# Kernel tuning notes

Hardware: AMD Instinct MI355X
Metric: run time of the kernel (lower is better)

Reference implementation:

```python
import jax, jax.numpy as jnp
import numpy as np

N_NODES = 50000
N_EDGES = 800000
IN_C = 128
OUT_C = 128
EDGE_F = 16
NEG_SLOPE = 0.2
BN_EPS = 1e-5


def setup_inputs() -> dict:
    key = jax.random.key(0)
    ks = jax.random.split(key, 8)
    x = jax.random.normal(ks[0], (N_NODES, IN_C), dtype=jnp.float32)
    edge_index = jax.random.randint(ks[1], (2, N_EDGES), 0, N_NODES, dtype=jnp.int64)
    edge_attr = jax.random.normal(ks[2], (N_EDGES, EDGE_F), dtype=jnp.float32)
    W = jax.random.normal(ks[3], (IN_C, OUT_C), dtype=jnp.float32) / np.sqrt(IN_C)
    att_src = jax.random.normal(ks[4], (OUT_C,), dtype=jnp.float32) / np.sqrt(OUT_C)
    att_dst = jax.random.normal(ks[5], (OUT_C,), dtype=jnp.float32) / np.sqrt(OUT_C)
    bias = jnp.zeros((OUT_C,), dtype=jnp.float32)
    gamma = jnp.ones((OUT_C,), dtype=jnp.float32)
    beta = jnp.zeros((OUT_C,), dtype=jnp.float32)
    return {"x": x, "edge_index": edge_index, "edge_attr": edge_attr, "W": W,
            "att_src": att_src, "att_dst": att_dst, "bias": bias,
            "gamma": gamma, "beta": beta}


def reference(x, edge_index, edge_attr, W, att_src, att_dst, bias, gamma, beta):
    # GATConv, heads=1, concat=False; edge_attr is ignored (edge_dim=None in original).
    N = x.shape[0]
    h = x @ W  # [N, C] linear projection (shared lin_src/lin_dst)
    # add self loops (PyG default add_self_loops=True)
    loops = jnp.broadcast_to(jnp.arange(N, dtype=edge_index.dtype)[None, :], (2, N))
    ei = jnp.concatenate([edge_index, loops], axis=1)
    src, dst = ei[0], ei[1]
    a_src = h @ att_src  # [N] per-node source attention logit
    a_dst = h @ att_dst  # [N] per-node target attention logit
    e = jax.nn.leaky_relu(a_src[src] + a_dst[dst], NEG_SLOPE)  # [E+N]
    # segment softmax over edges grouped by destination node
    m = jax.ops.segment_max(e, dst, num_segments=N)  # every node has a self loop -> nonempty
    ex = jnp.exp(e - m[dst])
    denom = jax.ops.segment_sum(ex, dst, num_segments=N)
    alpha = ex / denom[dst]  # [E+N]
    out = jax.ops.segment_sum(alpha[:, None] * h[src], dst, num_segments=N) + bias  # [N, C]
    # NodeLevelBatchNorm in training mode: batch stats over nodes, biased variance
    mean = jnp.mean(out, axis=0)
    var = jnp.mean((out - mean) ** 2, axis=0)
    y = (out - mean) * jax.lax.rsqrt(var + BN_EPS) * gamma + beta
    return jax.nn.relu(y)
```

## Files before the change

### kernel.cpp

```cpp
#include <hip/hip_runtime.h>
#include <hip/hip_bf16.h>

#define NN 50000
#define NE 800000
#define NC 128
#define NEG 0.2f
#define BN_EPS 1e-5f
#define NB 391
#define EPB 2048
#define DEPTH 16
#define CAP 2560
#define CAPR 2688
#define GB 391
#define AGGB 2048

typedef unsigned int u32;
typedef unsigned short u16;
typedef short bf16x8 __attribute__((ext_vector_type(8)));
typedef float f32x4 __attribute__((ext_vector_type(4)));

#define OFF_H       0
#define OFF_ACCUM   3200000
#define OFF_ASRC    6400000
#define OFF_ADST    6450000
#define OFF_GCUR    6500000
#define OFF_GSUM    6500512
#define OFF_GSUMSQ  6500640
#define OFF_BEG     6500768
#define OFF_ENDA    6550768
#define OFF_WINV    6600768
#define OFF_BIN     6650768
#define OFF_REC     7651728
#define OFF_WB      9753744
#define OFF_PS      9761936
#define OFF_PQ      10024080
#define OFF_WSEND   10286224
#define NZERO       512

__device__ __forceinline__ float leaky(float e) { return (e >= 0.f) ? e : NEG * e; }

__device__ __forceinline__ u16 f2b(float f) {
  union { float f; u32 u; } v; v.f = f;
  u32 u = v.u;
  return (u16)((u + 0x7fffu + ((u >> 16) & 1u)) >> 16);
}
__device__ __forceinline__ float blo(u32 u) {
  union { u32 u; float f; } v; v.u = u << 16; return v.f;
}
__device__ __forceinline__ float bhi(u32 u) {
  union { u32 u; float f; } v; v.u = u & 0xffff0000u; return v.f;
}

__device__ __forceinline__ bool ei_is64(const void* ei_raw) {
  const unsigned long long* p64 = (const unsigned long long*)ei_raw;
  bool is64 = true;
#pragma unroll
  for (int k = 0; k < 8; ++k) is64 = is64 && (p64[k] < (unsigned long long)NN);
  return is64;
}

__global__ __launch_bounds__(256) void k_prep(
    const float* __restrict__ W, u32* __restrict__ Wb32, int* __restrict__ zbase) {
  if (blockIdx.x == 0) {
    for (int i = threadIdx.x; i < NZERO; i += 256) zbase[i] = 0;
  }
  int q = blockIdx.x * 256 + threadIdx.x;
  if (q >= 2048) return;
  int f = q >> 6, l = q & 63;
  int n = f >> 2, s = f & 3;
  int col = 16 * n + (l & 15);
  int kb = 32 * s + 8 * (l >> 4);
#pragma unroll
  for (int j2 = 0; j2 < 4; ++j2) {
    u16 e0 = f2b(W[(kb + 2 * j2) * NC + col]);
    u16 e1 = f2b(W[(kb + 2 * j2 + 1) * NC + col]);
    Wb32[q * 4 + j2] = ((u32)e1 << 16) | e0;
  }
}

__global__ __launch_bounds__(256) void k_gemm_bin(
    const float* __restrict__ x, const u16* __restrict__ Wb,
    const float* __restrict__ attS, const float* __restrict__ attD,
    u16* __restrict__ h, float* __restrict__ a_src, float* __restrict__ a_dst,
    const void* __restrict__ ei_raw, int* __restrict__ gcur, u32* __restrict__ bin) {
  __shared__ int cnt[NB];
  __shared__ u32 buf[NB * DEPTH];
  const int t = threadIdx.x;

  if (blockIdx.x >= GB) {
    for (int i = t; i < NB; i += 256) cnt[i] = 0;
    __syncthreads();
    bool is64 = ei_is64(ei_raw);
    int base = (blockIdx.x - GB) * EPB;
#pragma unroll
    for (int k = 0; k < 8; ++k) {
      int idx = base + k * 256 + t;
      if (idx >= NE) continue;
      int s, d;
      if (is64) {
        s = (int)((const long long*)ei_raw)[idx];
        d = (int)((const long long*)ei_raw)[NE + idx];
      } else {
        s = ((const int*)ei_raw)[idx];
        d = ((const int*)ei_raw)[NE + idx];
      }
      int b = d >> 7;
      u32 pack = (u32)s | ((u32)(d & 127) << 16);
      int p = atomicAdd(&cnt[b], 1);
      if (p < DEPTH) buf[b * DEPTH + p] = pack;
      else {
        int g = atomicAdd(&gcur[b], 1);
        if (g < CAP) bin[b * CAP + g] = pack;
      }
    }
    __syncthreads();
    for (int b = t; b < NB; b += 256) {
      int c = min(cnt[b], DEPTH);
      if (c > 0) {
        int g = atomicAdd(&gcur[b], c);
        int lim = min(c, max(0, CAP - g));
        int gp = b * CAP + g;
#pragma unroll 4
        for (int i = 0; i < lim; ++i) bin[gp + i] = buf[b * DEPTH + i];
      }
    }
    return;
  }

  const int l = t & 63;
  const int r0 = blockIdx.x * 128 + (t >> 6) * 32;
  const int lr = l & 15;
  const int kg = l >> 4;

  f32x4 acc[2][8];
#pragma unroll
  for (int t2 = 0; t2 < 2; ++t2)
#pragma unroll
    for (int n = 0; n < 8; ++n) acc[t2][n] = (f32x4){0.f, 0.f, 0.f, 0.f};

#pragma unroll
  for (int s = 0; s < 4; ++s) {
    bf16x8 bfr[8];
#pragma unroll
    for (int n = 0; n < 8; ++n)
      bfr[n] = *(const bf16x8*)(Wb + ((size_t)((n * 4 + s) * 64 + l)) * 8);

#pragma unroll
    for (int t2 = 0; t2 < 2; ++t2) {
      int arow = r0 + t2 * 16 + lr;
      f32x4 a0 = (f32x4){0.f,0.f,0.f,0.f}, a1 = a0;
      if (arow < NN) {
        const float* xa = x + (size_t)arow * NC + kg * 8 + s * 32;
        a0 = *(const f32x4*)xa;
        a1 = *(const f32x4*)(xa + 4);
      }
      bf16x8 af;
      af[0]=(short)f2b(a0[0]); af[1]=(short)f2b(a0[1]);
      af[2]=(short)f2b(a0[2]); af[3]=(short)f2b(a0[3]);
      af[4]=(short)f2b(a1[0]); af[5]=(short)f2b(a1[1]);
      af[6]=(short)f2b(a1[2]); af[7]=(short)f2b(a1[3]);
#pragma unroll
      for (int n = 0; n < 8; ++n)
        acc[t2][n] = __builtin_amdgcn_mfma_f32_16x16x32_bf16(af, bfr[n], acc[t2][n], 0, 0, 0);
    }
  }

  float attS_r[8], attD_r[8];
#pragma unroll
  for (int n = 0; n < 8; ++n) {
    attS_r[n] = attS[16 * n + lr];
    attD_r[n] = attD[16 * n + lr];
  }
#pragma unroll
  for (int t2 = 0; t2 < 2; ++t2) {
#pragma unroll
    for (int q = 0; q < 4; ++q) {
      int row = r0 + t2 * 16 + kg * 4 + q;
      bool rok = row < NN;
      float sA = 0.f, sD = 0.f;
#pragma unroll
      for (int n = 0; n < 8; ++n) {
        float v = acc[t2][n][q];
        sA += v * attS_r[n];
        sD += v * attD_r[n];
        if (rok) h[(size_t)row * NC + 16 * n + lr] = f2b(v);
      }
      sA += __shfl_xor(sA, 1); sD += __shfl_xor(sD, 1);
      sA += __shfl_xor(sA, 2); sD += __shfl_xor(sD, 2);
      sA += __shfl_xor(sA, 4); sD += __shfl_xor(sD, 4);
      sA += __shfl_xor(sA, 8); sD += __shfl_xor(sD, 8);
      if (lr == 0 && rok) { a_src[row] = sA; a_dst[row] = sD; }
    }
  }
}

__global__ __launch_bounds__(256) void k_build(
    const int* __restrict__ gcur, const u32* __restrict__ bin,
    const float* __restrict__ a_src, const float* __restrict__ a_dst,
    int* __restrict__ begA, int* __restrict__ endA, float* __restrict__ winv,
    u32* __restrict__ rec) {
  __shared__ int cnt[128], bs[128], cur[128];
  __shared__ float aDl[128], wsh[128];
  int t = threadIdx.x;
  int b = blockIdx.x;
  int nbase = b << 7;
  int nmax = min(128, NN - nbase);
  int ebeg = b * CAP;
  int rbeg = b * CAPR;
  int E = min(gcur[b], CAP);
  if (t < 128) {
    cnt[t] = 0; wsh[t] = 0.f;
    if (t < nmax) aDl[t] = a_dst[nbase + t];
  }
  __syncthreads();
  for (int i = t; i < E; i += 256)
    atomicAdd(&cnt[bin[ebeg + i] >> 16], 1);
  __syncthreads();
  if (t < 128) bs[t] = cnt[t];
  __syncthreads();
  for (int off = 1; off < 128; off <<= 1) {
    int xv = (t < 128 && t >= off) ? bs[t - off] : 0;
    __syncthreads();
    if (t < 128) bs[t] += xv;
    __syncthreads();
  }
  if (t < 128) {
    bs[t] -= cnt[t];
    cur[t] = 0;
  }
  __syncthreads();
  for (int i = t; i < E; i += 256) {
    u32 e = bin[ebeg + i];
    int s = e & 0xFFFF;
    int ld = e >> 16;
    int p = atomicAdd(&cur[ld], 1);
    int pos = rbeg + bs[ld] + ld + p;
    float w = __expf(leaky(a_src[s] + aDl[ld]));
    rec[2 * pos] = (u32)s;
    rec[2 * pos + 1] = __float_as_uint(w);
    atomicAdd(&wsh[ld], w);
  }
  __syncthreads();
  if (t < nmax) {
    int node = nbase + t;
    int bg = rbeg + bs[t] + t;
    int cn = cnt[t];
    float wself = __expf(leaky(a_src[node] + aDl[t]));
    rec[2 * (bg + cn)] = (u32)node;
    rec[2 * (bg + cn) + 1] = __float_as_uint(wself);
    begA[node] = bg;
    endA[node] = bg + cn + 1;
    winv[node] = 1.f / (wsh[t] + wself);
  }
}

__global__ __launch_bounds__(256) void k_aggregate(
    const int* __restrict__ begA, const int* __restrict__ endA,
    const u32* __restrict__ rec, const float* __restrict__ winv,
    const u16* __restrict__ h, u32* __restrict__ accum,
    float* __restrict__ partS, float* __restrict__ partQ) {
  int t = threadIdx.x;
  int l = t & 63;
  int wv = t >> 6;
  const u32* h32 = (const u32*)h;
  const uint2* rec2 = (const uint2*)rec;
  float cs0 = 0.f, cs1 = 0.f, cq0 = 0.f, cq1 = 0.f;

#define P1(EJ, A)                                                          \
  {                                                                        \
    int sj = __builtin_amdgcn_readfirstlane((int)(EJ).x);                  \
    float wj = __uint_as_float((EJ).y);                                    \
    u32 g = h32[(size_t)sj * 64 + l];                                      \
    A.x += wj * blo(g);                                                    \
    A.y += wj * bhi(g);                                                    \
  }

  for (int d = blockIdx.x * 4 + wv; d < NN; d += AGGB * 4) {
    int beg = __builtin_amdgcn_readfirstlane(begA[d]);
    int end = __builtin_amdgcn_readfirstlane(endA[d]);

    float2 a0 = make_float2(0.f, 0.f), a1 = a0, a2 = a0, a3 = a0;
    int j = beg;
    for (; j + 8 <= end; j += 8) {
      const uint2* rp = rec2 + j;
      uint2 e0 = rp[0], e1 = rp[1], e2 = rp[2], e3 = rp[3];
      uint2 e4 = rp[4], e5 = rp[5], e6 = rp[6], e7 = rp[7];
      P1(e0, a0) P1(e1, a1) P1(e2, a2) P1(e3, a3)
      P1(e4, a0) P1(e5, a1) P1(e6, a2) P1(e7, a3)
    }
    for (; j + 2 <= end; j += 2) {
      uint2 e0 = rec2[j], e1 = rec2[j + 1];
      P1(e0, a0) P1(e1, a1)
    }
    if (j < end) {
      uint2 e0 = rec2[j];
      P1(e0, a0)
    }

    float inv = winv[d];
    float ox = (a0.x + a1.x + a2.x + a3.x) * inv;
    float oy = (a0.y + a1.y + a2.y + a3.y) * inv;
    accum[(size_t)d * 64 + l] = ((u32)f2b(oy) << 16) | f2b(ox);
    cs0 += ox; cs1 += oy;
    cq0 += ox * ox; cq1 += oy * oy;
  }
#undef P1

  __shared__ float2 shS[256], shQ[256];
  shS[t] = make_float2(cs0, cs1);
  shQ[t] = make_float2(cq0, cq1);
  __syncthreads();
  if (t < 64) {
    float2 a = shS[t], b = shQ[t];
#pragma unroll
    for (int g = 1; g < 4; ++g) {
      float2 s2v = shS[g * 64 + t], q2 = shQ[g * 64 + t];
      a.x += s2v.x; a.y += s2v.y;
      b.x += q2.x;  b.y += q2.y;
    }
    partS[blockIdx.x * 128 + 2 * t]     = a.x;
    partS[blockIdx.x * 128 + 2 * t + 1] = a.y;
    partQ[blockIdx.x * 128 + 2 * t]     = b.x;
    partQ[blockIdx.x * 128 + 2 * t + 1] = b.y;
  }
}

__global__ __launch_bounds__(256) void k_stats2(
    const float* __restrict__ partS, const float* __restrict__ partQ,
    float* __restrict__ gsum, float* __restrict__ gsumsq) {
  __shared__ float shw[4];
  int t = threadIdx.x;
  int b = blockIdx.x;
  int c = b & 127;
  const float* src = (b >> 7) ? partQ : partS;
  float a = 0.f;
#pragma unroll
  for (int i = t; i < AGGB; i += 256) a += src[(size_t)i * 128 + c];
  for (int off = 32; off > 0; off >>= 1) a += __shfl_xor(a, off);
  if ((t & 63) == 0) shw[t >> 6] = a;
  __syncthreads();
  if (t == 0) {
    float r = shw[0] + shw[1] + shw[2] + shw[3];
    if (b >> 7) gsumsq[c] = r;
    else        gsum[c] = r;
  }
}

__global__ __launch_bounds__(256) void k_bn(
    const u32* __restrict__ accum, const float* __restrict__ gsum,
    const float* __restrict__ gsumsq, const float* __restrict__ gamma,
    const float* __restrict__ beta, float* __restrict__ out) {
  int i4 = blockIdx.x * 256 + threadIdx.x;
  if (i4 >= NN * NC / 4) return;
  int c4 = (i4 * 4) & 127;
  f32x4 gs = *(const f32x4*)&gsum[c4];
  f32x4 gq = *(const f32x4*)&gsumsq[c4];
  f32x4 ga = *(const f32x4*)&gamma[c4];
  f32x4 be = *(const f32x4*)&beta[c4];
  u32 p0 = accum[(size_t)i4 * 2];
  u32 p1 = accum[(size_t)i4 * 2 + 1];
  f32x4 v = (f32x4){blo(p0), bhi(p0), blo(p1), bhi(p1)};
  f32x4 o;
#pragma unroll
  for (int j = 0; j < 4; ++j) {
    float mean = gs[j] * (1.0f / NN);
    float var = gq[j] * (1.0f / NN) - mean * mean;
    float inv = rsqrtf(var + BN_EPS);
    float y = (v[j] - mean) * inv * ga[j] + be[j];
    o[j] = (y > 0.f) ? y : 0.f;
  }
  *(f32x4*)&out[(size_t)i4 * 4] = o;
}

extern "C" void kernel_launch(void* const* d_in, const int* in_sizes, int n_in,
                              void* d_out, int out_size, void* d_ws, size_t ws_size,
                              hipStream_t stream) {
  const float* x    = (const float*)d_in[0];
  const void*  ei   = d_in[1];
  const float* W    = (const float*)d_in[3];
  const float* attS = (const float*)d_in[4];
  const float* attD = (const float*)d_in[5];
  const float* gamma = (const float*)d_in[7];
  const float* beta  = (const float*)d_in[8];

  float* ws     = (float*)d_ws;
  u16*   h      = (u16*)(ws + OFF_H);
  u32*   accum  = (u32*)(ws + OFF_ACCUM);
  float* a_src  = ws + OFF_ASRC;
  float* a_dst  = ws + OFF_ADST;
  int*   gcur   = (int*)(ws + OFF_GCUR);
  float* gsum   = ws + OFF_GSUM;
  float* gsumsq = ws + OFF_GSUMSQ;
  int*   begA   = (int*)(ws + OFF_BEG);
  int*   endA   = (int*)(ws + OFF_ENDA);
  float* winv   = ws + OFF_WINV;
  u32*   bin    = (u32*)(ws + OFF_BIN);
  u32*   rec    = (u32*)(ws + OFF_REC);
  u32*   wb32   = (u32*)(ws + OFF_WB);
  float* partS  = ws + OFF_PS;
  float* partQ  = ws + OFF_PQ;

  const int nbin = (NE + EPB - 1) / EPB;
  k_prep<<<8, 256, 0, stream>>>(W, wb32, gcur);
  k_gemm_bin<<<GB + nbin, 256, 0, stream>>>(x, (const u16*)wb32, attS, attD,
                                            h, a_src, a_dst, ei, gcur, bin);
  k_build<<<NB, 256, 0, stream>>>(gcur, bin, a_src, a_dst, begA, endA, winv, rec);
  k_aggregate<<<AGGB, 256, 0, stream>>>(begA, endA, rec, winv, h,
                                        accum, partS, partQ);
  k_stats2<<<256, 256, 0, stream>>>(partS, partQ, gsum, gsumsq);
  k_bn<<<(NN * NC / 4 + 255) / 256, 256, 0, stream>>>(accum, gsum, gsumsq, gamma, beta,
                                                      (float*)d_out);
}
```

Before: 90.93 us.

## Split aggregation into channel slices with edge-parallel lanes per wave

The aggregate kernel now splits the 128 channels into 8 slices of 16, one slice per block. Each wave handles one destination node with 8 edges in flight per iteration (8 lanes per edge, 8 channel pairs), then combines the partial sums with shuffles. Accumulators are stored slice-major, and the stats and BN kernels are adapted to that layout. The aim is to cut per-block h traffic to a smaller channel window for better cache locality and to expose more edge-level memory parallelism. In exchange, the edge records are re-read once per slice and the row reads become narrow 32-byte gathers.

New measurement: 176.1 us. 93.6% more time.

```diff
diff --git a/kernel.cpp b/kernel.cpp
--- a/kernel.cpp
+++ b/kernel.cpp
@@ -33,8 +33,8 @@
 #define OFF_REC     7651728
 #define OFF_WB      9753744
 #define OFF_PS      9761936
-#define OFF_PQ      10024080
-#define OFF_WSEND   10286224
+#define OFF_PQ      9794704
+#define OFF_WSEND   9827472
 #define NZERO       512
 
 __device__ __forceinline__ float leaky(float e) { return (e >= 0.f) ? e : NEG * e; }
@@ -262,66 +262,61 @@
   int t = threadIdx.x;
   int l = t & 63;
   int wv = t >> 6;
+  int eidx = l >> 3;
+  int cp = l & 7;
+  int slice = blockIdx.x & 7;
+  int sblk = blockIdx.x >> 3;
+  int sbase = slice * 8;
   const u32* h32 = (const u32*)h;
   const uint2* rec2 = (const uint2*)rec;
+  u32* accS = accum + (size_t)slice * NN * 8;
   float cs0 = 0.f, cs1 = 0.f, cq0 = 0.f, cq1 = 0.f;
 
-#define P1(EJ, A)                                                          \
-  {                                                                        \
-    int sj = __builtin_amdgcn_readfirstlane((int)(EJ).x);                  \
-    float wj = __uint_as_float((EJ).y);                                    \
-    u32 g = h32[(size_t)sj * 64 + l];                                      \
-    A.x += wj * blo(g);                                                    \
-    A.y += wj * bhi(g);                                                    \
-  }
-
-  for (int d = blockIdx.x * 4 + wv; d < NN; d += AGGB * 4) {
-    int beg = __builtin_amdgcn_readfirstlane(begA[d]);
-    int end = __builtin_amdgcn_readfirstlane(endA[d]);
-
-    float2 a0 = make_float2(0.f, 0.f), a1 = a0, a2 = a0, a3 = a0;
-    int j = beg;
-    for (; j + 8 <= end; j += 8) {
-      const uint2* rp = rec2 + j;
-      uint2 e0 = rp[0], e1 = rp[1], e2 = rp[2], e3 = rp[3];
-      uint2 e4 = rp[4], e5 = rp[5], e6 = rp[6], e7 = rp[7];
-      P1(e0, a0) P1(e1, a1) P1(e2, a2) P1(e3, a3)
-      P1(e4, a0) P1(e5, a1) P1(e6, a2) P1(e7, a3)
-    }
-    for (; j + 2 <= end; j += 2) {
-      uint2 e0 = rec2[j], e1 = rec2[j + 1];
-      P1(e0, a0) P1(e1, a1)
-    }
-    if (j < end) {
-      uint2 e0 = rec2[j];
-      P1(e0, a0)
-    }
-
+  for (int d = sblk * 4 + wv; d < NN; d += 1024) {
+    int beg = begA[d], end = endA[d];
     float inv = winv[d];
-    float ox = (a0.x + a1.x + a2.x + a3.x) * inv;
-    float oy = (a0.y + a1.y + a2.y + a3.y) * inv;
-    accum[(size_t)d * 64 + l] = ((u32)f2b(oy) << 16) | f2b(ox);
+    float2 aA = make_float2(0.f, 0.f), aB = aA;
+    for (int j = beg; j < end; j += 16) {
+      int rem = end - j;
+      if (eidx < rem) {
+        uint2 e = rec2[j + eidx];
+        u32 g = h32[(size_t)e.x * 64 + sbase + cp];
+        float w = __uint_as_float(e.y);
+        aA.x += w * blo(g);
+        aA.y += w * bhi(g);
+      }
+      if (eidx + 8 < rem) {
+        uint2 e = rec2[j + 8 + eidx];
+        u32 g = h32[(size_t)e.x * 64 + sbase + cp];
+        float w = __uint_as_float(e.y);
+        aB.x += w * blo(g);
+        aB.y += w * bhi(g);
+      }
+    }
+    float ax = aA.x + aB.x, ay = aA.y + aB.y;
+    ax += __shfl_xor(ax, 8);  ay += __shfl_xor(ay, 8);
+    ax += __shfl_xor(ax, 16); ay += __shfl_xor(ay, 16);
+    ax += __shfl_xor(ax, 32); ay += __shfl_xor(ay, 32);
+    float ox = ax * inv, oy = ay * inv;
+    if (eidx == 0) accS[(size_t)d * 8 + cp] = ((u32)f2b(oy) << 16) | f2b(ox);
     cs0 += ox; cs1 += oy;
     cq0 += ox * ox; cq1 += oy * oy;
   }
-#undef P1
-
-  __shared__ float2 shS[256], shQ[256];
-  shS[t] = make_float2(cs0, cs1);
-  shQ[t] = make_float2(cq0, cq1);
-  __syncthreads();
-  if (t < 64) {
-    float2 a = shS[t], b = shQ[t];
+
+  __shared__ float4 shP[4][8];
+  if (eidx == 0) shP[wv][cp] = make_float4(cs0, cs1, cq0, cq1);
+  __syncthreads();
+  if (t < 8) {
+    float4 a = shP[0][t];
 #pragma unroll
     for (int g = 1; g < 4; ++g) {
-      float2 s2v = shS[g * 64 + t], q2 = shQ[g * 64 + t];
-      a.x += s2v.x; a.y += s2v.y;
-      b.x += q2.x;  b.y += q2.y;
-    }
-    partS[blockIdx.x * 128 + 2 * t]     = a.x;
-    partS[blockIdx.x * 128 + 2 * t + 1] = a.y;
-    partQ[blockIdx.x * 128 + 2 * t]     = b.x;
-    partQ[blockIdx.x * 128 + 2 * t + 1] = b.y;
+      float4 b = shP[g][t];
+      a.x += b.x; a.y += b.y; a.z += b.z; a.w += b.w;
+    }
+    partS[blockIdx.x * 16 + 2 * t]     = a.x;
+    partS[blockIdx.x * 16 + 2 * t + 1] = a.y;
+    partQ[blockIdx.x * 16 + 2 * t]     = a.z;
+    partQ[blockIdx.x * 16 + 2 * t + 1] = a.w;
   }
 }
 
@@ -332,10 +327,9 @@
   int t = threadIdx.x;
   int b = blockIdx.x;
   int c = b & 127;
+  int slice = c >> 4, j = c & 15;
   const float* src = (b >> 7) ? partQ : partS;
-  float a = 0.f;
-#pragma unroll
-  for (int i = t; i < AGGB; i += 256) a += src[(size_t)i * 128 + c];
+  float a = src[(size_t)(8 * t + slice) * 16 + j];
   for (int off = 32; off > 0; off >>= 1) a += __shfl_xor(a, off);
   if ((t & 63) == 0) shw[t >> 6] = a;
   __syncthreads();
@@ -352,13 +346,18 @@
     const float* __restrict__ beta, float* __restrict__ out) {
   int i4 = blockIdx.x * 256 + threadIdx.x;
   if (i4 >= NN * NC / 4) return;
-  int c4 = (i4 * 4) & 127;
+  int d = i4 >> 5;
+  int ci = i4 & 31;
+  int c4 = ci * 4;
+  int slice = ci >> 2;
+  int off = (ci & 3) * 2;
   f32x4 gs = *(const f32x4*)&gsum[c4];
   f32x4 gq = *(const f32x4*)&gsumsq[c4];
   f32x4 ga = *(const f32x4*)&gamma[c4];
   f32x4 be = *(const f32x4*)&beta[c4];
-  u32 p0 = accum[(size_t)i4 * 2];
-  u32 p1 = accum[(size_t)i4 * 2 + 1];
+  const u32* accS = accum + (size_t)slice * NN * 8 + (size_t)d * 8 + off;
+  u32 p0 = accS[0];
+  u32 p1 = accS[1];
   f32x4 v = (f32x4){blo(p0), bhi(p0), blo(p1), bhi(p1)};
   f32x4 o;
 #pragma unroll
```
